# Kernel tuning notes

Measured on AMD Instinct MI355X. Metric: run time of the kernel, lower is better.

## Reference

```python
import jax, jax.numpy as jnp
import numpy as np

Q, C, T = 256, 128, 128
L = Q + C + T            # 512
D = 1024                 # d_model
H = 8                    # heads
DK = D // H              # 128 = self_attn.d_k
F = 3                    # num_latent_relations
R = 50                   # num_relation_kinds = len(relations2id)
FF = 4 * D               # feed-forward hidden
DEFAULT_QQ_ID = 0        # relations2id['q:q-default']
EPS = 1e-5


def setup_inputs():
    key = jax.random.key(0)
    ks = jax.random.split(key, 40)
    s = 0.02
    def nrm(k, shape, scale=s):
        return jax.random.normal(k, shape, jnp.float32) * scale
    inp = {
        'x': jax.random.normal(ks[0], (1, L, D), jnp.float32),
        'qc_relation': jax.random.uniform(ks[1], (Q, C, F), jnp.float32),
        'cq_relation': jax.random.uniform(ks[2], (C, Q, F), jnp.float32),
        'qt_relation': jax.random.uniform(ks[3], (Q, T, F), jnp.float32),
        'tq_relation': jax.random.uniform(ks[4], (T, Q, F), jnp.float32),
        'ct_relation': jax.random.randint(ks[5], (C + T, C + T), 0, R, jnp.int32),
        'predefined_relation': jax.random.randint(ks[6], (L, L), 0, R, jnp.int32),
        'mask': jnp.ones((1, L, L), jnp.int32),
        # relation embedding tables
        'rel_k_emb': nrm(ks[7], (R, DK)), 'rel_v_emb': nrm(ks[8], (R, DK)),
        'lqc_k': nrm(ks[9], (F, DK)), 'lqc_v': nrm(ks[10], (F, DK)),
        'lcq_k': nrm(ks[11], (F, DK)), 'lcq_v': nrm(ks[12], (F, DK)),
        'lqt_k': nrm(ks[13], (F, DK)), 'lqt_v': nrm(ks[14], (F, DK)),
        'ltq_k': nrm(ks[15], (F, DK)), 'ltq_v': nrm(ks[16], (F, DK)),
        # attention projections (torch Linear: y = x @ W.T + b)
        'Wq': nrm(ks[17], (D, D)), 'bq': jnp.zeros((D,), jnp.float32),
        'Wk': nrm(ks[18], (D, D)), 'bk': jnp.zeros((D,), jnp.float32),
        'Wv': nrm(ks[19], (D, D)), 'bv': jnp.zeros((D,), jnp.float32),
        'Wo': nrm(ks[20], (D, D)), 'bo': jnp.zeros((D,), jnp.float32),
        # layer norms
        'ln1_g': jnp.ones((D,), jnp.float32), 'ln1_b': jnp.zeros((D,), jnp.float32),
        'ln2_g': jnp.ones((D,), jnp.float32), 'ln2_b': jnp.zeros((D,), jnp.float32),
        # FFN
        'W1': nrm(ks[21], (FF, D)), 'b1': jnp.zeros((FF,), jnp.float32),
        'W2': nrm(ks[22], (D, FF)), 'b2': jnp.zeros((D,), jnp.float32),
    }
    return inp


def layer_norm(x, g, b):
    m = jnp.mean(x, -1, keepdims=True)
    v = jnp.mean((x - m) ** 2, -1, keepdims=True)
    return (x - m) * jax.lax.rsqrt(v + EPS) * g + b


def build_latent_relation(ct, qc, cq, qt, tq, emb, lqc, lcq, lqt, ltq):
    # qq block: every entry is the default-qq embedding row
    qq = jnp.broadcast_to(emb[DEFAULT_QQ_ID], (Q, Q, DK))
    qc_e = jnp.einsum('qcf,fd->qcd', qc, lqc)
    cq_e = jnp.einsum('cqf,fd->cqd', cq, lcq)
    qt_e = jnp.einsum('qtf,fd->qtd', qt, lqt)
    tq_e = jnp.einsum('tqf,fd->tqd', tq, ltq)
    ct_e = emb[ct]                                      # [(c+t),(c+t),DK]
    top = jnp.concatenate([qq, qc_e, qt_e], axis=1)      # [Q, L, DK]
    bot = jnp.concatenate([jnp.concatenate([cq_e, tq_e], 0), ct_e], axis=1)  # [C+T, L, DK]
    return jnp.concatenate([top, bot], axis=0)           # [L, L, DK]


def relation_attention(x, rel_k, rel_v, mask, Wq, bq, Wk, bk, Wv, bv, Wo, bo):
    B = x.shape[0]
    def proj(W, b):
        return (x @ W.T + b).reshape(B, L, H, DK).transpose(0, 2, 1, 3)  # [B,H,L,DK]
    q, k, v = proj(Wq, bq), proj(Wk, bk), proj(Wv, bv)
    scores = (jnp.einsum('bhid,bhjd->bhij', q, k)
              + jnp.einsum('bhid,ijd->bhij', q, rel_k)) / jnp.sqrt(jnp.float32(DK))
    scores = jnp.where(mask[:, None] == 0, jnp.float32(-1e9), scores)
    p = jax.nn.softmax(scores, axis=-1)
    o = (jnp.einsum('bhij,bhjd->bhid', p, v)
         + jnp.einsum('bhij,ijd->bhid', p, rel_v))
    o = o.transpose(0, 2, 1, 3).reshape(B, L, D)
    return o @ Wo.T + bo


def reference(x, qc_relation, cq_relation, qt_relation, tq_relation,
              ct_relation, predefined_relation, mask,
              rel_k_emb, rel_v_emb, lqc_k, lqc_v, lcq_k, lcq_v,
              lqt_k, lqt_v, ltq_k, ltq_v,
              Wq, bq, Wk, bk, Wv, bv, Wo, bo,
              ln1_g, ln1_b, ln2_g, ln2_b, W1, b1, W2, b2):
    # latent relation build + combine with predefined lookup
    rel_k = (rel_k_emb[predefined_relation]
             + build_latent_relation(ct_relation, qc_relation, cq_relation,
                                     qt_relation, tq_relation,
                                     rel_k_emb, lqc_k, lcq_k, lqt_k, ltq_k))
    rel_v = (rel_v_emb[predefined_relation]
             + build_latent_relation(ct_relation, qc_relation, cq_relation,
                                     qt_relation, tq_relation,
                                     rel_v_emb, lqc_v, lcq_v, lqt_v, ltq_v))
    # sublayer 0: pre-norm relation-biased self attention (dropout=0)
    h = x + relation_attention(layer_norm(x, ln1_g, ln1_b), rel_k, rel_v, mask,
                               Wq, bq, Wk, bk, Wv, bv, Wo, bo)
    # sublayer 1: pre-norm FFN
    y = layer_norm(h, ln2_g, ln2_b)
    ffn = jax.nn.relu(y @ W1.T + b1) @ W2.T + b2
    return h + ffn
```

## Files before the change

### kernel.cpp

```cpp
#include <hip/hip_runtime.h>
#include <hip/hip_bf16.h>

#define LL 512
#define DD 1024
#define HH 8
#define DKK 128
#define QQ 256
#define CCC 128
#define TTT 128
#define RR 50
#define FFF 4096

typedef __attribute__((ext_vector_type(8))) short short8;
typedef __attribute__((ext_vector_type(4))) float float4v;

__device__ __forceinline__ unsigned short f2bu(float f) {
  __hip_bfloat16 h = __float2bfloat16(f);
  unsigned short u; __builtin_memcpy(&u, &h, 2); return u;
}
__device__ __forceinline__ float b2f(unsigned short u) {
  unsigned int v = ((unsigned int)u) << 16;
  float f; __builtin_memcpy(&f, &v, 4); return f;
}
__device__ __forceinline__ int4 cvt8(float4 x, float4 y) {
  int4 o;
  o.x = (int)f2bu(x.x) | ((int)f2bu(x.y) << 16);
  o.y = (int)f2bu(x.z) | ((int)f2bu(x.w) << 16);
  o.z = (int)f2bu(y.x) | ((int)f2bu(y.y) << 16);
  o.w = (int)f2bu(y.z) | ((int)f2bu(y.w) << 16);
  return o;
}

__device__ __forceinline__ void lds_barrier() {
  __builtin_amdgcn_sched_barrier(0);
  __builtin_amdgcn_s_waitcnt(0xC07F);
  __builtin_amdgcn_s_barrier();
  __builtin_amdgcn_sched_barrier(0);
}

#define LOADSET(A0,A1,B0,B1,F0,F1,F2,F3,itv) { int k0v = (itv) << 6;          \
  A0 = *(const int4*)(Az + (size_t)(bm + r)*lda + k0v + gc*8);                \
  A1 = *(const int4*)(Az + (size_t)(bm + 32 + r)*lda + k0v + gc*8);           \
  if constexpr (!CONVB) {                                                     \
    B0 = *(const int4*)(Bz16 + (size_t)(bnb + r)*ldb + k0v + gc*8);           \
    if constexpr (NB > 1)                                                     \
      B1 = *(const int4*)(Bz16 + (size_t)(bnb + 32 + r)*ldb + k0v + gc*8);    \
  } else {                                                                    \
    F0 = *(const float4*)(Bz32 + (size_t)(bnb + r)*ldb + k0v + gc*8);         \
    F1 = *(const float4*)(Bz32 + (size_t)(bnb + r)*ldb + k0v + gc*8 + 4);     \
    if constexpr (NB > 1) {                                                   \
      F2 = *(const float4*)(Bz32 + (size_t)(bnb + 32 + r)*ldb + k0v + gc*8);  \
      F3 = *(const float4*)(Bz32 + (size_t)(bnb + 32 + r)*ldb + k0v + gc*8 + 4); } } }

#define STORESET2(basep,A0,A1,B0,B1,F0,F1,F2,F3) {                            \
  char* bse = (basep);                                                        \
  *(int4*)(bse + r*128 + sl*16) = A0;                                         \
  *(int4*)(bse + (32 + r)*128 + sl*16) = A1;                                  \
  if constexpr (!CONVB) {                                                     \
    *(int4*)(bse + ABYTES + r*128 + sl*16) = B0;                              \
    if constexpr (NB > 1)                                                     \
      *(int4*)(bse + ABYTES + (32 + r)*128 + sl*16) = B1;                     \
  } else {                                                                    \
    *(int4*)(bse + ABYTES + r*128 + sl*16) = cvt8(F0, F1);                    \
    if constexpr (NB > 1)                                                     \
      *(int4*)(bse + ABYTES + (32 + r)*128 + sl*16) = cvt8(F2, F3); } }

__global__ __launch_bounds__(256) void ln_bf16_kernel(const float* __restrict__ x,
    const float* __restrict__ g, const float* __restrict__ b,
    unsigned short* __restrict__ y)
{
  int row = blockIdx.x, t = threadIdx.x;
  const float4 xv = ((const float4*)(x + row*DD))[t];
  float s  = xv.x+xv.y+xv.z+xv.w;
  float ss = xv.x*xv.x+xv.y*xv.y+xv.z*xv.z+xv.w*xv.w;
  __shared__ float rs[256], rss[256];
  rs[t]=s; rss[t]=ss; __syncthreads();
  for (int st=128; st>0; st>>=1){ if (t<st){ rs[t]+=rs[t+st]; rss[t]+=rss[t+st]; } __syncthreads(); }
  float mean = rs[0] * (1.0f/DD);
  float var  = rss[0]*(1.0f/DD) - mean*mean;
  float inv  = rsqrtf(var + 1e-5f);
  float4 gv = ((const float4*)g)[t], bv = ((const float4*)b)[t];
  ushort4 ov;
  ov.x = f2bu((xv.x-mean)*inv*gv.x + bv.x);
  ov.y = f2bu((xv.y-mean)*inv*gv.y + bv.y);
  ov.z = f2bu((xv.z-mean)*inv*gv.z + bv.z);
  ov.w = f2bu((xv.w-mean)*inv*gv.w + bv.w);
  ((ushort4*)(y + row*DD))[t] = ov;
}

__global__ __launch_bounds__(256) void ln_bf16_addb_kernel(float* __restrict__ x,
    const float* __restrict__ g, const float* __restrict__ b,
    const float* __restrict__ b2, unsigned short* __restrict__ y)
{
  int row = blockIdx.x, t = threadIdx.x;
  const float4 xv = ((const float4*)(x + row*DD))[t];
  float s  = xv.x+xv.y+xv.z+xv.w;
  float ss = xv.x*xv.x+xv.y*xv.y+xv.z*xv.z+xv.w*xv.w;
  __shared__ float rs[256], rss[256];
  rs[t]=s; rss[t]=ss; __syncthreads();
  for (int st=128; st>0; st>>=1){ if (t<st){ rs[t]+=rs[t+st]; rss[t]+=rss[t+st]; } __syncthreads(); }
  float mean = rs[0] * (1.0f/DD);
  float var  = rss[0]*(1.0f/DD) - mean*mean;
  float inv  = rsqrtf(var + 1e-5f);
  float4 gv = ((const float4*)g)[t], bv = ((const float4*)b)[t];
  ushort4 ov;
  ov.x = f2bu((xv.x-mean)*inv*gv.x + bv.x);
  ov.y = f2bu((xv.y-mean)*inv*gv.y + bv.y);
  ov.z = f2bu((xv.z-mean)*inv*gv.z + bv.z);
  ov.w = f2bu((xv.w-mean)*inv*gv.w + bv.w);
  ((ushort4*)(y + row*DD))[t] = ov;
  float4 b2v = ((const float4*)b2)[t];
  float4 nx; nx.x = xv.x+b2v.x; nx.y = xv.y+b2v.y; nx.z = xv.z+b2v.z; nx.w = xv.w+b2v.w;
  ((float4*)(x + row*DD))[t] = nx;
}

template<int BN, int CONVB, int ZK, int OUT_BF16, int RELU, int HAS_SRC, int HAS_BIAS>
__global__ __launch_bounds__(256) void gemm_pl(
    const unsigned short* __restrict__ A, int lda, size_t sAz,
    const void* __restrict__ Bv, int ldb, size_t sBz,
    const float* __restrict__ bias,
    const float* __restrict__ src, int ldsrc, size_t sSz,
    void* __restrict__ Cv, int ldc, size_t sCz,
    int K)
{
  constexpr int BM = 64;
  constexpr int WM = 32, WN = BN/2, FM = 2, FN = WN/16;
  constexpr int NB = BN/32;
  constexpr int ABYTES = BM*128, TILE = ABYTES + BN*128;
  __shared__ char lds[2*TILE];
  int t = threadIdx.x, w = t >> 6, l = t & 63;
  size_t z = blockIdx.z;
  const unsigned short* Az = A + z*sAz;
  const unsigned short* Bz16 = (const unsigned short*)Bv + (CONVB ? 0 : z*sBz);
  const float*          Bz32 = (const float*)Bv + (CONVB ? z*sBz : 0);
  int bm = blockIdx.y*BM, bn = blockIdx.x*BN;
  int bnb = bn;
  int wm = (w>>1)*WM, wn = (w&1)*WN;

  float4v acc[FM][FN];
  #pragma unroll
  for (int m=0;m<FM;++m)
    #pragma unroll
    for (int n=0;n<FN;++n) acc[m][n] = (float4v){0.f,0.f,0.f,0.f};

  int r = t >> 3, sl = t & 7;
  int gc = sl ^ (r & 7);
  int quad = l >> 4, lrow = l & 15;
  const int nit = K >> 6;

  int4 pa0, pa1, pb0, pb1;  float4 pf0, pf1, pf2, pf3;
  int4 qa0, qa1, qb0, qb1;  float4 qf0, qf1, qf2, qf3;

  auto compute = [&](const char* base) {
    const char* ab = base;
    const char* bb = base + ABYTES;
    #pragma unroll
    for (int step=0; step<2; ++step) {
      int c = step*4 + quad;
      short8 af[FM], bf[FN];
      #pragma unroll
      for (int m=0;m<FM;++m) {
        int Rw = wm + m*16 + lrow;
        af[m] = *(const short8*)(ab + Rw*128 + ((c ^ (Rw & 7))*16));
      }
      #pragma unroll
      for (int n=0;n<FN;++n) {
        int Rw = wn + n*16 + lrow;
        bf[n] = *(const short8*)(bb + Rw*128 + ((c ^ (Rw & 7))*16));
      }
      #pragma unroll
      for (int m=0;m<FM;++m)
        #pragma unroll
        for (int n=0;n<FN;++n)
          acc[m][n] = __builtin_amdgcn_mfma_f32_16x16x32_bf16(af[m], bf[n], acc[m][n], 0, 0, 0);
    }
  };

  LOADSET(pa0,pa1,pb0,pb1,pf0,pf1,pf2,pf3, 0);
  LOADSET(qa0,qa1,qb0,qb1,qf0,qf1,qf2,qf3, 1);
  for (int it = 0; it < nit; it += 2) {
    STORESET2(lds, pa0,pa1,pb0,pb1,pf0,pf1,pf2,pf3);
    if (it + 2 < nit) LOADSET(pa0,pa1,pb0,pb1,pf0,pf1,pf2,pf3, it+2);
    lds_barrier();
    compute(lds);
    STORESET2(lds + TILE, qa0,qa1,qb0,qb1,qf0,qf1,qf2,qf3);
    if (it + 3 < nit) LOADSET(qa0,qa1,qb0,qb1,qf0,qf1,qf2,qf3, it+3);
    lds_barrier();
    compute(lds + TILE);
  }

  #pragma unroll
  for (int m=0;m<FM;++m)
    #pragma unroll
    for (int n=0;n<FN;++n)
      #pragma unroll
      for (int rg=0;rg<4;++rg) {
        int row = bm + wm + m*16 + quad*4 + rg;
        int col = bn + wn + n*16 + lrow;
        float vv = acc[m][n][rg];
        if (ZK) {
          atomicAdd(&((float*)Cv)[(size_t)row*ldc + col], vv);
        } else {
          if (HAS_BIAS) vv += bias[col];
          if (HAS_SRC)  vv += src[z*sSz + (size_t)row*ldsrc + col];
          if (RELU) vv = fmaxf(vv, 0.f);
          if (OUT_BF16) ((unsigned short*)Cv)[z*sCz + (size_t)row*ldc + col] = f2bu(vv);
          else          ((float*)Cv)[z*sCz + (size_t)row*ldc + col] = vv;
        }
      }
}

__global__ __launch_bounds__(256) void gemm_qkv_pl(
    const unsigned short* __restrict__ A,
    const float* __restrict__ Wq, const float* __restrict__ Wk,
    const float* __restrict__ Wv,
    const float* __restrict__ bq, const float* __restrict__ bk,
    const float* __restrict__ bv,
    unsigned short* __restrict__ Qh, unsigned short* __restrict__ Kh,
    unsigned short* __restrict__ Vt)
{
  constexpr int BN = 64, CONVB = 1;
  constexpr int WM = 32, WN = 32, FM = 2, FN = 2;
  constexpr int NB = 2;
  constexpr int ABYTES = 64*128, TILE = ABYTES + BN*128;
  __shared__ char lds[2*TILE];
  int t = threadIdx.x, w = t >> 6, l = t & 63;
  int bm = blockIdx.y*64, bn = blockIdx.x*BN;
  int wm = (w>>1)*WM, wn = (w&1)*WN;
  const int lda = DD, ldb = DD, nit = DD >> 6;
  const unsigned short* Az = A;
  int part0 = bn >> 10;
  const float* Bz32 = (part0==0 ? Wq : part0==1 ? Wk : Wv) + (size_t)(bn & 1023)*DD;
  const unsigned short* Bz16 = nullptr; (void)Bz16;
  int bnb = 0;

  float4v acc[FM][FN];
  #pragma unroll
  for (int m=0;m<FM;++m)
    #pragma unroll
    for (int n=0;n<FN;++n) acc[m][n] = (float4v){0.f,0.f,0.f,0.f};

  int r = t >> 3, sl = t & 7;
  int gc = sl ^ (r & 7);
  int quad = l >> 4, lrow = l & 15;

  int4 pa0, pa1, pb0, pb1;  float4 pf0, pf1, pf2, pf3;
  int4 qa0, qa1, qb0, qb1;  float4 qf0, qf1, qf2, qf3;

  auto compute = [&](const char* base) {
    const char* ab = base;
    const char* bb = base + ABYTES;
    #pragma unroll
    for (int step=0; step<2; ++step) {
      int c = step*4 + quad;
      short8 af[FM], bf[FN];
      #pragma unroll
      for (int m=0;m<FM;++m) {
        int Rw = wm + m*16 + lrow;
        af[m] = *(const short8*)(ab + Rw*128 + ((c ^ (Rw & 7))*16));
      }
      #pragma unroll
      for (int n=0;n<FN;++n) {
        int Rw = wn + n*16 + lrow;
        bf[n] = *(const short8*)(bb + Rw*128 + ((c ^ (Rw & 7))*16));
      }
      #pragma unroll
      for (int m=0;m<FM;++m)
        #pragma unroll
        for (int n=0;n<FN;++n)
          acc[m][n] = __builtin_amdgcn_mfma_f32_16x16x32_bf16(af[m], bf[n], acc[m][n], 0, 0, 0);
    }
  };

  LOADSET(pa0,pa1,pb0,pb1,pf0,pf1,pf2,pf3, 0);
  LOADSET(qa0,qa1,qb0,qb1,qf0,qf1,qf2,qf3, 1);
  for (int it = 0; it < nit; it += 2) {
    STORESET2(lds, pa0,pa1,pb0,pb1,pf0,pf1,pf2,pf3);
    if (it + 2 < nit) LOADSET(pa0,pa1,pb0,pb1,pf0,pf1,pf2,pf3, it+2);
    lds_barrier();
    compute(lds);
    STORESET2(lds + TILE, qa0,qa1,qb0,qb1,qf0,qf1,qf2,qf3);
    if (it + 3 < nit) LOADSET(qa0,qa1,qb0,qb1,qf0,qf1,qf2,qf3, it+3);
    lds_barrier();
    compute(lds + TILE);
  }

  #pragma unroll
  for (int m=0;m<FM;++m)
    #pragma unroll
    for (int n=0;n<FN;++n)
      #pragma unroll
      for (int rg=0;rg<4;++rg) {
        int row = bm + wm + m*16 + quad*4 + rg;
        int col = bn + wn + n*16 + lrow;
        int part = col >> 10, hh = (col >> 7) & 7, d = col & 127;
        const float* bp = (part==0) ? bq : (part==1) ? bk : bv;
        float vv = acc[m][n][rg] + bp[col & 1023];
        unsigned short o = f2bu(vv);
        if (part == 0)      Qh[((size_t)hh*LL + row)*DKK + d] = o;
        else if (part == 1) Kh[((size_t)hh*LL + row)*DKK + d] = o;
        else                Vt[((size_t)hh*DKK + d)*LL + row] = o;
      }
}

__global__ __launch_bounds__(64) void qtab_kernel(const unsigned short* __restrict__ Qh,
    const float* __restrict__ embk,
    const float* __restrict__ lqc, const float* __restrict__ lqt,
    const float* __restrict__ lcq, const float* __restrict__ ltq,
    float* __restrict__ qe, float* __restrict__ ql)
{
  int i = blockIdx.x, h = blockIdx.y, t = threadIdx.x;
  __shared__ float qrow[128];
  const unsigned short* qp = Qh + ((size_t)h*LL + i)*DKK;
  qrow[t] = b2f(qp[t]); qrow[t+64] = b2f(qp[t+64]);
  __syncthreads();
  if (t < RR) {
    float s = 0.f;
    #pragma unroll 8
    for (int d=0; d<128; ++d) s += qrow[d]*embk[t*128+d];
    qe[(i*HH+h)*RR + t] = s;
  } else if (t < RR + 12) {
    int u = t - RR;
    int tb = u/3, f = u - tb*3;
    const float* tab = (tb==0) ? lqc : (tb==1) ? lqt : (tb==2) ? lcq : ltq;
    const float* tr = tab + f*128;
    float s = 0.f;
    #pragma unroll 8
    for (int d=0; d<128; ++d) s += qrow[d]*tr[d];
    ql[((tb*LL + i)*HH + h)*3 + f] = s;
  }
}

__global__ __launch_bounds__(512) void softmax_pw_kernel(
    float* __restrict__ S,
    const float* __restrict__ qe, const float* __restrict__ ql,
    const float* __restrict__ qcr, const float* __restrict__ cqr,
    const float* __restrict__ qtr, const float* __restrict__ tqr,
    const int* __restrict__ ct,   const int* __restrict__ pred,
    const int* __restrict__ mask,
    const float* __restrict__ embv,
    const float* __restrict__ lqc_v, const float* __restrict__ lcq_v,
    const float* __restrict__ lqt_v, const float* __restrict__ ltq_v,
    float* __restrict__ o2)
{
  int i = blockIdx.x, h = blockIdx.y, j = threadIdx.x;
  int w = j >> 6;
  __shared__ float qerow[52];
  __shared__ float pws[52];
  __shared__ float pf1s[3], pf2s[3];
  __shared__ float redw[8], redw2[8];
  if (j < RR) qerow[j] = qe[(i*HH+h)*RR + j];
  if (j >= 64 && j < 64+52) pws[j-64] = 0.f;
  if (j >= 192 && j < 195) pf1s[j-192] = 0.f;
  if (j >= 256 && j < 259) pf2s[j-256] = 0.f;

  float lq1[3] = {0,0,0}, lq2[3] = {0,0,0};
  if (i < QQ) {
    #pragma unroll
    for (int f=0; f<3; ++f) {
      lq1[f] = ql[((0*LL + i)*HH + h)*3 + f];
      lq2[f] = ql[((1*LL + i)*HH + h)*3 + f];
    }
  } else if (i < QQ+CCC) {
    #pragma unroll
    for (int f=0; f<3; ++f) lq1[f] = ql[((2*LL + i)*HH + h)*3 + f];
  } else {
    #pragma unroll
    for (int f=0; f<3; ++f) lq1[f] = ql[((3*LL + i)*HH + h)*3 + f];
  }

  float c0=0.f, c1=0.f, c2=0.f; int route; int scat2 = 0;
  if (i < QQ) {
    if (j < QQ) { route = 0; scat2 = 0; }
    else if (j < QQ+CCC) { const float* rr = qcr + (i*CCC + (j-QQ))*3;
      c0=rr[0]; c1=rr[1]; c2=rr[2]; route = 1; }
    else { const float* rr = qtr + (i*TTT + (j-QQ-CCC))*3;
      c0=rr[0]; c1=rr[1]; c2=rr[2]; route = 2; }
  } else {
    if (j < QQ) { const float* rr = (i < QQ+CCC) ? cqr + ((i-QQ)*QQ + j)*3
                                                 : tqr + ((i-QQ-CCC)*QQ + j)*3;
      c0=rr[0]; c1=rr[1]; c2=rr[2]; route = 1; }
    else { route = 0; scat2 = ct[(i-QQ)*(CCC+TTT) + (j-QQ)]; }
  }
  int predv = pred[i*LL + j];
  float s = S[((size_t)h*LL + i)*LL + j];
  __syncthreads();

  s += qerow[predv];
  if (route == 0)      s += qerow[scat2];
  else if (route == 1) s += c0*lq1[0] + c1*lq1[1] + c2*lq1[2];
  else                 s += c0*lq2[0] + c1*lq2[1] + c2*lq2[2];
  s *= 0.08838834764831845f;
  if (mask[i*LL + j] == 0) s = -1e9f;

  float m = s;
  #pragma unroll
  for (int off=32; off>=1; off>>=1) m = fmaxf(m, __shfl_xor(m, off));
  if ((j & 63) == 0) redw[w] = m;
  __syncthreads();
  float mx = redw[0];
  #pragma unroll
  for (int k=1; k<8; ++k) mx = fmaxf(mx, redw[k]);

  float e = __expf(s - mx);
  float sm = e;
  #pragma unroll
  for (int off=32; off>=1; off>>=1) sm += __shfl_xor(sm, off);
  if ((j & 63) == 0) redw2[w] = sm;
  __syncthreads();
  float tot = 0.f;
  #pragma unroll
  for (int k=0; k<8; ++k) tot += redw2[k];
  float p = e * (1.0f/tot);

  ((unsigned short*)S)[((size_t)h*LL + i)*1024 + j] = f2bu(p);

  atomicAdd(&pws[predv], p);
  if (route == 0) atomicAdd(&pws[scat2], p);
  float f10=0.f,f11=0.f,f12=0.f,f20=0.f,f21=0.f,f22=0.f;
  if (route == 1) { f10=p*c0; f11=p*c1; f12=p*c2; }
  else if (route == 2) { f20=p*c0; f21=p*c1; f22=p*c2; }
  #pragma unroll
  for (int off=32; off>=1; off>>=1) {
    f10 += __shfl_xor(f10, off); f11 += __shfl_xor(f11, off); f12 += __shfl_xor(f12, off);
    f20 += __shfl_xor(f20, off); f21 += __shfl_xor(f21, off); f22 += __shfl_xor(f22, off);
  }
  if ((j & 63) == 0) {
    atomicAdd(&pf1s[0], f10); atomicAdd(&pf1s[1], f11); atomicAdd(&pf1s[2], f12);
    atomicAdd(&pf2s[0], f20); atomicAdd(&pf2s[1], f21); atomicAdd(&pf2s[2], f22);
  }
  __syncthreads();

  if (j < 128) {
    const float* tab1; const float* tab2 = nullptr;
    if (i < QQ)          { tab1 = lqc_v; tab2 = lqt_v; }
    else if (i < QQ+CCC) { tab1 = lcq_v; }
    else                 { tab1 = ltq_v; }
    int d = j;
    float acc = 0.f;
    #pragma unroll 5
    for (int r = 0; r < RR; ++r) acc += pws[r]*embv[r*128 + d];
    acc += pf1s[0]*tab1[d] + pf1s[1]*tab1[128+d] + pf1s[2]*tab1[256+d];
    if (tab2) acc += pf2s[0]*tab2[d] + pf2s[1]*tab2[128+d] + pf2s[2]*tab2[256+d];
    o2[((size_t)h*LL + i)*DKK + d] = acc;
  }
}

extern "C" void kernel_launch(void* const* d_in, const int* in_sizes, int n_in,
                              void* d_out, int out_size, void* d_ws, size_t ws_size,
                              hipStream_t stream)
{
  const float* x    = (const float*)d_in[0];
  const float* qcr  = (const float*)d_in[1];
  const float* cqr  = (const float*)d_in[2];
  const float* qtr  = (const float*)d_in[3];
  const float* tqr  = (const float*)d_in[4];
  const int*   ct   = (const int*)d_in[5];
  const int*   pred = (const int*)d_in[6];
  const int*   mask = (const int*)d_in[7];
  const float* embk = (const float*)d_in[8];
  const float* embv = (const float*)d_in[9];
  const float* lqc_k = (const float*)d_in[10];
  const float* lqc_v = (const float*)d_in[11];
  const float* lcq_k = (const float*)d_in[12];
  const float* lcq_v = (const float*)d_in[13];
  const float* lqt_k = (const float*)d_in[14];
  const float* lqt_v = (const float*)d_in[15];
  const float* ltq_k = (const float*)d_in[16];
  const float* ltq_v = (const float*)d_in[17];
  const float* Wq = (const float*)d_in[18]; const float* bq = (const float*)d_in[19];
  const float* Wk = (const float*)d_in[20]; const float* bk = (const float*)d_in[21];
  const float* Wv = (const float*)d_in[22]; const float* bv = (const float*)d_in[23];
  const float* Wo = (const float*)d_in[24]; const float* bo = (const float*)d_in[25];
  const float* ln1_g = (const float*)d_in[26]; const float* ln1_b = (const float*)d_in[27];
  const float* ln2_g = (const float*)d_in[28]; const float* ln2_b = (const float*)d_in[29];
  const float* W1 = (const float*)d_in[30]; const float* b1 = (const float*)d_in[31];
  const float* W2 = (const float*)d_in[32]; const float* b2 = (const float*)d_in[33];
  float* out = (float*)d_out;

  float* wsf = (float*)d_ws;
  float* S    = wsf;
  float* o2   = S + (size_t)HH*LL*LL;
  float* qe   = o2 + (size_t)HH*LL*DKK;
  float* ql   = qe + LL*HH*RR;
  unsigned short* ub = (unsigned short*)(ql + 4*LL*HH*3);
  unsigned short* ybuf_b = ub;
  unsigned short* obuf_b = ybuf_b + LL*DD;
  unsigned short* Qh     = obuf_b + LL*DD;
  unsigned short* Kh     = Qh + LL*DD;
  unsigned short* Vt     = Kh + LL*DD;
  unsigned short* PS     = (unsigned short*)S;
  unsigned short* hidden = (unsigned short*)S;

  ln_bf16_kernel<<<LL, 256, 0, stream>>>(x, ln1_g, ln1_b, ybuf_b);
  gemm_qkv_pl<<<dim3(48, 8), 256, 0, stream>>>(ybuf_b, Wq, Wk, Wv, bq, bk, bv,
                                               Qh, Kh, Vt);
  qtab_kernel<<<dim3(LL, HH), 64, 0, stream>>>(Qh, embk, lqc_k, lqt_k, lcq_k, ltq_k, qe, ql);
  gemm_pl<64,0,0,0,0,0,0><<<dim3(8, 8, 8), 256, 0, stream>>>(
      Qh, DKK, (size_t)LL*DKK, Kh, DKK, (size_t)LL*DKK,
      nullptr, nullptr, 0, 0, S, LL, (size_t)LL*LL, DKK);
  softmax_pw_kernel<<<dim3(LL, HH), 512, 0, stream>>>(
      S, qe, ql, qcr, cqr, qtr, tqr, ct, pred, mask,
      embv, lqc_v, lcq_v, lqt_v, ltq_v, o2);
  gemm_pl<32,0,0,1,0,1,0><<<dim3(4, 8, 8), 256, 0, stream>>>(
      PS, 1024, (size_t)LL*1024, Vt, LL, (size_t)DKK*LL,
      nullptr, o2, DKK, (size_t)LL*DKK, obuf_b, DD, (size_t)DKK, LL);
  gemm_pl<32,1,0,0,0,1,1><<<dim3(32, 8, 1), 256, 0, stream>>>(
      obuf_b, DD, 0, Wo, DD, 0, bo, x, DD, 0, out, DD, 0, DD);
  ln_bf16_addb_kernel<<<LL, 256, 0, stream>>>(out, ln2_g, ln2_b, b2, ybuf_b);
  gemm_pl<64,1,0,1,1,0,1><<<dim3(64, 8, 1), 256, 0, stream>>>(
      ybuf_b, DD, 0, W1, DD, 0, b1, nullptr, 0, 0, hidden, FFF, 0, DD);
  gemm_pl<64,1,1,0,0,0,0><<<dim3(16, 8, 4), 256, 0, stream>>>(
      hidden, FFF, (size_t)1024, W2, FFF, (size_t)1024,
      nullptr, nullptr, 0, 0, out, DD, 0, 1024);
}
```

Before: 276.7 us.

## Fold relation-key tables into QK GEMM, batch heads in softmax, deepen prefetch

Appends the relation key embedding and latent tables as 64 extra rows of each head's K buffer, so the QK^T GEMM also produces the q·emb scores. This removes the separate qtab kernel and its qe/ql buffers. The softmax kernel now handles all 8 heads per row in one block, which amortises the pred/mask/relation loads across heads. Most GEMMs also get a 4-deep register prefetch pipeline, at the cost of more registers and a changed workspace layout (padded S/PS strides).

```diff
diff --git a/kernel.cpp b/kernel.cpp
--- a/kernel.cpp
+++ b/kernel.cpp
@@ -10,6 +10,9 @@
 #define TTT 128
 #define RR 50
 #define FFF 4096
+#define KLD 576
+#define SLD 576
+#define PLD 1152
 
 typedef __attribute__((ext_vector_type(8))) short short8;
 typedef __attribute__((ext_vector_type(4))) float float4v;
@@ -64,6 +67,25 @@
     *(int4*)(bse + ABYTES + r*128 + sl*16) = cvt8(F0, F1);                    \
     if constexpr (NB > 1)                                                     \
       *(int4*)(bse + ABYTES + (32 + r)*128 + sl*16) = cvt8(F2, F3); } }
+
+__global__ __launch_bounds__(256) void kprep_kernel(
+    const float* __restrict__ embk,
+    const float* __restrict__ lqc, const float* __restrict__ lqt,
+    const float* __restrict__ lcq, const float* __restrict__ ltq,
+    unsigned short* __restrict__ Kh)
+{
+  int g = blockIdx.x*256 + threadIdx.x;
+  if (g >= 8*64*128) return;
+  int d = g & 127, rr = (g >> 7) & 63, h = g >> 13;
+  float v = 0.f;
+  if (rr < 50) v = embk[rr*128 + d];
+  else if (rr < 62) {
+    int u = rr - 50; int tb = u/3, f = u - tb*3;
+    const float* tab = (tb==0) ? lqc : (tb==1) ? lqt : (tb==2) ? lcq : ltq;
+    v = tab[f*128 + d];
+  }
+  Kh[((size_t)h*KLD + 512 + rr)*DKK + d] = f2bu(v);
+}
 
 __global__ __launch_bounds__(256) void ln_bf16_kernel(const float* __restrict__ x,
     const float* __restrict__ g, const float* __restrict__ b,
@@ -114,7 +136,7 @@
   ((float4*)(x + row*DD))[t] = nx;
 }
 
-template<int BN, int CONVB, int ZK, int OUT_BF16, int RELU, int HAS_SRC, int HAS_BIAS>
+template<int BN, int DEPTH, int CONVB, int ZK, int OUT_BF16, int RELU, int HAS_SRC, int HAS_BIAS>
 __global__ __launch_bounds__(256) void gemm_pl(
     const unsigned short* __restrict__ A, int lda, size_t sAz,
     const void* __restrict__ Bv, int ldb, size_t sBz,
@@ -148,8 +170,10 @@
   int quad = l >> 4, lrow = l & 15;
   const int nit = K >> 6;
 
-  int4 pa0, pa1, pb0, pb1;  float4 pf0, pf1, pf2, pf3;
-  int4 qa0, qa1, qb0, qb1;  float4 qf0, qf1, qf2, qf3;
+  int4 Aa0, Aa1, Ab0, Ab1;  float4 Af0, Af1, Af2, Af3;
+  int4 Ba0, Ba1, Bb0, Bb1;  float4 Bf0, Bf1, Bf2, Bf3;
+  int4 Ca0, Ca1, Cb0, Cb1;  float4 Cf0, Cf1, Cf2, Cf3;
+  int4 Da0, Da1, Db0, Db1;  float4 Df0, Df1, Df2, Df3;
 
   auto compute = [&](const char* base) {
     const char* ab = base;
@@ -176,17 +200,42 @@
     }
   };
 
-  LOADSET(pa0,pa1,pb0,pb1,pf0,pf1,pf2,pf3, 0);
-  LOADSET(qa0,qa1,qb0,qb1,qf0,qf1,qf2,qf3, 1);
-  for (int it = 0; it < nit; it += 2) {
-    STORESET2(lds, pa0,pa1,pb0,pb1,pf0,pf1,pf2,pf3);
-    if (it + 2 < nit) LOADSET(pa0,pa1,pb0,pb1,pf0,pf1,pf2,pf3, it+2);
-    lds_barrier();
-    compute(lds);
-    STORESET2(lds + TILE, qa0,qa1,qb0,qb1,qf0,qf1,qf2,qf3);
-    if (it + 3 < nit) LOADSET(qa0,qa1,qb0,qb1,qf0,qf1,qf2,qf3, it+3);
-    lds_barrier();
-    compute(lds + TILE);
+  if constexpr (DEPTH == 2) {
+    LOADSET(Aa0,Aa1,Ab0,Ab1,Af0,Af1,Af2,Af3, 0);
+    LOADSET(Ba0,Ba1,Bb0,Bb1,Bf0,Bf1,Bf2,Bf3, 1);
+    for (int it = 0; it < nit; it += 2) {
+      STORESET2(lds, Aa0,Aa1,Ab0,Ab1,Af0,Af1,Af2,Af3);
+      if (it + 2 < nit) LOADSET(Aa0,Aa1,Ab0,Ab1,Af0,Af1,Af2,Af3, it+2);
+      lds_barrier();
+      compute(lds);
+      STORESET2(lds + TILE, Ba0,Ba1,Bb0,Bb1,Bf0,Bf1,Bf2,Bf3);
+      if (it + 3 < nit) LOADSET(Ba0,Ba1,Bb0,Bb1,Bf0,Bf1,Bf2,Bf3, it+3);
+      lds_barrier();
+      compute(lds + TILE);
+    }
+  } else {
+    LOADSET(Aa0,Aa1,Ab0,Ab1,Af0,Af1,Af2,Af3, 0);
+    LOADSET(Ba0,Ba1,Bb0,Bb1,Bf0,Bf1,Bf2,Bf3, 1);
+    LOADSET(Ca0,Ca1,Cb0,Cb1,Cf0,Cf1,Cf2,Cf3, 2);
+    LOADSET(Da0,Da1,Db0,Db1,Df0,Df1,Df2,Df3, 3);
+    for (int it = 0; it < nit; it += 4) {
+      STORESET2(lds, Aa0,Aa1,Ab0,Ab1,Af0,Af1,Af2,Af3);
+      if (it + 4 < nit) LOADSET(Aa0,Aa1,Ab0,Ab1,Af0,Af1,Af2,Af3, it+4);
+      lds_barrier();
+      compute(lds);
+      STORESET2(lds + TILE, Ba0,Ba1,Bb0,Bb1,Bf0,Bf1,Bf2,Bf3);
+      if (it + 5 < nit) LOADSET(Ba0,Ba1,Bb0,Bb1,Bf0,Bf1,Bf2,Bf3, it+5);
+      lds_barrier();
+      compute(lds + TILE);
+      STORESET2(lds, Ca0,Ca1,Cb0,Cb1,Cf0,Cf1,Cf2,Cf3);
+      if (it + 6 < nit) LOADSET(Ca0,Ca1,Cb0,Cb1,Cf0,Cf1,Cf2,Cf3, it+6);
+      lds_barrier();
+      compute(lds);
+      STORESET2(lds + TILE, Da0,Da1,Db0,Db1,Df0,Df1,Df2,Df3);
+      if (it + 7 < nit) LOADSET(Da0,Da1,Db0,Db1,Df0,Df1,Df2,Df3, it+7);
+      lds_barrier();
+      compute(lds + TILE);
+    }
   }
 
   #pragma unroll
@@ -244,8 +293,10 @@
   int gc = sl ^ (r & 7);
   int quad = l >> 4, lrow = l & 15;
 
-  int4 pa0, pa1, pb0, pb1;  float4 pf0, pf1, pf2, pf3;
-  int4 qa0, qa1, qb0, qb1;  float4 qf0, qf1, qf2, qf3;
+  int4 Aa0, Aa1, Ab0, Ab1;  float4 Af0, Af1, Af2, Af3;
+  int4 Ba0, Ba1, Bb0, Bb1;  float4 Bf0, Bf1, Bf2, Bf3;
+  int4 Ca0, Ca1, Cb0, Cb1;  float4 Cf0, Cf1, Cf2, Cf3;
+  int4 Da0, Da1, Db0, Db1;  float4 Df0, Df1, Df2, Df3;
 
   auto compute = [&](const char* base) {
     const char* ab = base;
@@ -272,15 +323,25 @@
     }
   };
 
-  LOADSET(pa0,pa1,pb0,pb1,pf0,pf1,pf2,pf3, 0);
-  LOADSET(qa0,qa1,qb0,qb1,qf0,qf1,qf2,qf3, 1);
-  for (int it = 0; it < nit; it += 2) {
-    STORESET2(lds, pa0,pa1,pb0,pb1,pf0,pf1,pf2,pf3);
-    if (it + 2 < nit) LOADSET(pa0,pa1,pb0,pb1,pf0,pf1,pf2,pf3, it+2);
+  LOADSET(Aa0,Aa1,Ab0,Ab1,Af0,Af1,Af2,Af3, 0);
+  LOADSET(Ba0,Ba1,Bb0,Bb1,Bf0,Bf1,Bf2,Bf3, 1);
+  LOADSET(Ca0,Ca1,Cb0,Cb1,Cf0,Cf1,Cf2,Cf3, 2);
+  LOADSET(Da0,Da1,Db0,Db1,Df0,Df1,Df2,Df3, 3);
+  for (int it = 0; it < nit; it += 4) {
+    STORESET2(lds, Aa0,Aa1,Ab0,Ab1,Af0,Af1,Af2,Af3);
+    if (it + 4 < nit) LOADSET(Aa0,Aa1,Ab0,Ab1,Af0,Af1,Af2,Af3, it+4);
     lds_barrier();
     compute(lds);
-    STORESET2(lds + TILE, qa0,qa1,qb0,qb1,qf0,qf1,qf2,qf3);
-    if (it + 3 < nit) LOADSET(qa0,qa1,qb0,qb1,qf0,qf1,qf2,qf3, it+3);
+    STORESET2(lds + TILE, Ba0,Ba1,Bb0,Bb1,Bf0,Bf1,Bf2,Bf3);
+    if (it + 5 < nit) LOADSET(Ba0,Ba1,Bb0,Bb1,Bf0,Bf1,Bf2,Bf3, it+5);
+    lds_barrier();
+    compute(lds + TILE);
+    STORESET2(lds, Ca0,Ca1,Cb0,Cb1,Cf0,Cf1,Cf2,Cf3);
+    if (it + 6 < nit) LOADSET(Ca0,Ca1,Cb0,Cb1,Cf0,Cf1,Cf2,Cf3, it+6);
+    lds_barrier();
+    compute(lds);
+    STORESET2(lds + TILE, Da0,Da1,Db0,Db1,Df0,Df1,Df2,Df3);
+    if (it + 7 < nit) LOADSET(Da0,Da1,Db0,Db1,Df0,Df1,Df2,Df3, it+7);
     lds_barrier();
     compute(lds + TILE);
   }
@@ -298,42 +359,13 @@
         float vv = acc[m][n][rg] + bp[col & 1023];
         unsigned short o = f2bu(vv);
         if (part == 0)      Qh[((size_t)hh*LL + row)*DKK + d] = o;
-        else if (part == 1) Kh[((size_t)hh*LL + row)*DKK + d] = o;
+        else if (part == 1) Kh[((size_t)hh*KLD + row)*DKK + d] = o;
         else                Vt[((size_t)hh*DKK + d)*LL + row] = o;
       }
-}
-
-__global__ __launch_bounds__(64) void qtab_kernel(const unsigned short* __restrict__ Qh,
-    const float* __restrict__ embk,
-    const float* __restrict__ lqc, const float* __restrict__ lqt,
-    const float* __restrict__ lcq, const float* __restrict__ ltq,
-    float* __restrict__ qe, float* __restrict__ ql)
-{
-  int i = blockIdx.x, h = blockIdx.y, t = threadIdx.x;
-  __shared__ float qrow[128];
-  const unsigned short* qp = Qh + ((size_t)h*LL + i)*DKK;
-  qrow[t] = b2f(qp[t]); qrow[t+64] = b2f(qp[t+64]);
-  __syncthreads();
-  if (t < RR) {
-    float s = 0.f;
-    #pragma unroll 8
-    for (int d=0; d<128; ++d) s += qrow[d]*embk[t*128+d];
-    qe[(i*HH+h)*RR + t] = s;
-  } else if (t < RR + 12) {
-    int u = t - RR;
-    int tb = u/3, f = u - tb*3;
-    const float* tab = (tb==0) ? lqc : (tb==1) ? lqt : (tb==2) ? lcq : ltq;
-    const float* tr = tab + f*128;
-    float s = 0.f;
-    #pragma unroll 8
-    for (int d=0; d<128; ++d) s += qrow[d]*tr[d];
-    ql[((tb*LL + i)*HH + h)*3 + f] = s;
-  }
 }
 
 __global__ __launch_bounds__(512) void softmax_pw_kernel(
     float* __restrict__ S,
-    const float* __restrict__ qe, const float* __restrict__ ql,
     const float* __restrict__ qcr, const float* __restrict__ cqr,
     const float* __restrict__ qtr, const float* __restrict__ tqr,
     const int* __restrict__ ct,   const int* __restrict__ pred,
@@ -343,32 +375,27 @@
     const float* __restrict__ lqt_v, const float* __restrict__ ltq_v,
     float* __restrict__ o2)
 {
-  int i = blockIdx.x, h = blockIdx.y, j = threadIdx.x;
-  int w = j >> 6;
-  __shared__ float qerow[52];
-  __shared__ float pws[52];
-  __shared__ float pf1s[3], pf2s[3];
-  __shared__ float redw[8], redw2[8];
-  if (j < RR) qerow[j] = qe[(i*HH+h)*RR + j];
-  if (j >= 64 && j < 64+52) pws[j-64] = 0.f;
-  if (j >= 192 && j < 195) pf1s[j-192] = 0.f;
-  if (j >= 256 && j < 259) pf2s[j-256] = 0.f;
-
-  float lq1[3] = {0,0,0}, lq2[3] = {0,0,0};
-  if (i < QQ) {
-    #pragma unroll
-    for (int f=0; f<3; ++f) {
-      lq1[f] = ql[((0*LL + i)*HH + h)*3 + f];
-      lq2[f] = ql[((1*LL + i)*HH + h)*3 + f];
-    }
-  } else if (i < QQ+CCC) {
-    #pragma unroll
-    for (int f=0; f<3; ++f) lq1[f] = ql[((2*LL + i)*HH + h)*3 + f];
-  } else {
-    #pragma unroll
-    for (int f=0; f<3; ++f) lq1[f] = ql[((3*LL + i)*HH + h)*3 + f];
-  }
-
+  int i = blockIdx.x, j = threadIdx.x, w = j >> 6;
+  __shared__ float qerow8[8][52];
+  __shared__ float lq1s[8][3], lq2s[8][3];
+  __shared__ float pws[8][52];
+  __shared__ float pf1s[8][3], pf2s[8][3];
+  __shared__ float redm[8][8], reds[8][8];
+
+  for (int k = j; k < 8*52; k += 512) ((float*)pws)[k] = 0.f;
+  if (j < 24) { ((float*)pf1s)[j] = 0.f; ((float*)pf2s)[j] = 0.f; }
+  if (j < 400) {
+    int h = j / 50, rr = j - h*50;
+    qerow8[h][rr] = S[((size_t)(h*LL + i))*SLD + 512 + rr];
+  } else if (j >= 448 && j < 472) {
+    int u = j - 448; int h = u / 3, f = u - h*3;
+    int base = (i < QQ) ? 562 : (i < QQ+CCC) ? 568 : 571;
+    lq1s[h][f] = S[((size_t)(h*LL + i))*SLD + base + f];
+    lq2s[h][f] = (i < QQ) ? S[((size_t)(h*LL + i))*SLD + 565 + f] : 0.f;
+  }
+
+  int predv = pred[i*LL + j];
+  int maskv = mask[i*LL + j];
   float c0=0.f, c1=0.f, c2=0.f; int route; int scat2 = 0;
   if (i < QQ) {
     if (j < QQ) { route = 0; scat2 = 0; }
@@ -382,67 +409,118 @@
       c0=rr[0]; c1=rr[1]; c2=rr[2]; route = 1; }
     else { route = 0; scat2 = ct[(i-QQ)*(CCC+TTT) + (j-QQ)]; }
   }
-  int predv = pred[i*LL + j];
-  float s = S[((size_t)h*LL + i)*LL + j];
+
+  float sv[8];
+  #pragma unroll
+  for (int h=0; h<8; ++h) sv[h] = S[((size_t)(h*LL + i))*SLD + j];
   __syncthreads();
 
-  s += qerow[predv];
-  if (route == 0)      s += qerow[scat2];
-  else if (route == 1) s += c0*lq1[0] + c1*lq1[1] + c2*lq1[2];
-  else                 s += c0*lq2[0] + c1*lq2[1] + c2*lq2[2];
-  s *= 0.08838834764831845f;
-  if (mask[i*LL + j] == 0) s = -1e9f;
-
-  float m = s;
-  #pragma unroll
-  for (int off=32; off>=1; off>>=1) m = fmaxf(m, __shfl_xor(m, off));
-  if ((j & 63) == 0) redw[w] = m;
+  #pragma unroll
+  for (int h=0; h<8; ++h) {
+    float s = sv[h] + qerow8[h][predv];
+    if (route == 0)      s += qerow8[h][scat2];
+    else if (route == 1) s += c0*lq1s[h][0] + c1*lq1s[h][1] + c2*lq1s[h][2];
+    else                 s += c0*lq2s[h][0] + c1*lq2s[h][1] + c2*lq2s[h][2];
+    s *= 0.08838834764831845f;
+    if (maskv == 0) s = -1e9f;
+    sv[h] = s;
+  }
+
+  float mv[8];
+  #pragma unroll
+  for (int h=0; h<8; ++h) mv[h] = sv[h];
+  #pragma unroll
+  for (int off=32; off>=1; off>>=1) {
+    #pragma unroll
+    for (int h=0; h<8; ++h) mv[h] = fmaxf(mv[h], __shfl_xor(mv[h], off));
+  }
+  if ((j & 63) == 0) {
+    #pragma unroll
+    for (int h=0; h<8; ++h) redm[h][w] = mv[h];
+  }
   __syncthreads();
-  float mx = redw[0];
-  #pragma unroll
-  for (int k=1; k<8; ++k) mx = fmaxf(mx, redw[k]);
-
-  float e = __expf(s - mx);
-  float sm = e;
-  #pragma unroll
-  for (int off=32; off>=1; off>>=1) sm += __shfl_xor(sm, off);
-  if ((j & 63) == 0) redw2[w] = sm;
+  float ev[8];
+  #pragma unroll
+  for (int h=0; h<8; ++h) {
+    float mx = redm[h][0];
+    #pragma unroll
+    for (int k=1; k<8; ++k) mx = fmaxf(mx, redm[h][k]);
+    ev[h] = __expf(sv[h] - mx);
+  }
+  float sm[8];
+  #pragma unroll
+  for (int h=0; h<8; ++h) sm[h] = ev[h];
+  #pragma unroll
+  for (int off=32; off>=1; off>>=1) {
+    #pragma unroll
+    for (int h=0; h<8; ++h) sm[h] += __shfl_xor(sm[h], off);
+  }
+  if ((j & 63) == 0) {
+    #pragma unroll
+    for (int h=0; h<8; ++h) reds[h][w] = sm[h];
+  }
   __syncthreads();
-  float tot = 0.f;
-  #pragma unroll
-  for (int k=0; k<8; ++k) tot += redw2[k];
-  float p = e * (1.0f/tot);
-
-  ((unsigned short*)S)[((size_t)h*LL + i)*1024 + j] = f2bu(p);
-
-  atomicAdd(&pws[predv], p);
-  if (route == 0) atomicAdd(&pws[scat2], p);
-  float f10=0.f,f11=0.f,f12=0.f,f20=0.f,f21=0.f,f22=0.f;
-  if (route == 1) { f10=p*c0; f11=p*c1; f12=p*c2; }
-  else if (route == 2) { f20=p*c0; f21=p*c1; f22=p*c2; }
-  #pragma unroll
-  for (int off=32; off>=1; off>>=1) {
-    f10 += __shfl_xor(f10, off); f11 += __shfl_xor(f11, off); f12 += __shfl_xor(f12, off);
-    f20 += __shfl_xor(f20, off); f21 += __shfl_xor(f21, off); f22 += __shfl_xor(f22, off);
-  }
-  if ((j & 63) == 0) {
-    atomicAdd(&pf1s[0], f10); atomicAdd(&pf1s[1], f11); atomicAdd(&pf1s[2], f12);
-    atomicAdd(&pf2s[0], f20); atomicAdd(&pf2s[1], f21); atomicAdd(&pf2s[2], f22);
+  float pv[8];
+  #pragma unroll
+  for (int h=0; h<8; ++h) {
+    float tot = 0.f;
+    #pragma unroll
+    for (int k=0; k<8; ++k) tot += reds[h][k];
+    pv[h] = ev[h] * (1.0f/tot);
+    ((unsigned short*)S)[((size_t)(h*LL + i))*PLD + j] = f2bu(pv[h]);
+    atomicAdd(&pws[h][predv], pv[h]);
+    if (route == 0) atomicAdd(&pws[h][scat2], pv[h]);
+  }
+  if (route == 1) {
+    #pragma unroll
+    for (int h=0; h<8; ++h) {
+      float f0 = pv[h]*c0, f1 = pv[h]*c1, f2 = pv[h]*c2;
+      #pragma unroll
+      for (int off=32; off>=1; off>>=1) {
+        f0 += __shfl_xor(f0, off); f1 += __shfl_xor(f1, off); f2 += __shfl_xor(f2, off);
+      }
+      if ((j & 63) == 0) {
+        atomicAdd(&pf1s[h][0], f0); atomicAdd(&pf1s[h][1], f1); atomicAdd(&pf1s[h][2], f2);
+      }
+    }
+  } else if (route == 2) {
+    #pragma unroll
+    for (int h=0; h<8; ++h) {
+      float f0 = pv[h]*c0, f1 = pv[h]*c1, f2 = pv[h]*c2;
+      #pragma unroll
+      for (int off=32; off>=1; off>>=1) {
+        f0 += __shfl_xor(f0, off); f1 += __shfl_xor(f1, off); f2 += __shfl_xor(f2, off);
+      }
+      if ((j & 63) == 0) {
+        atomicAdd(&pf2s[h][0], f0); atomicAdd(&pf2s[h][1], f1); atomicAdd(&pf2s[h][2], f2);
+      }
+    }
   }
   __syncthreads();
 
-  if (j < 128) {
+  {
+    int h0 = j >> 7;
+    int d  = j & 127;
     const float* tab1; const float* tab2 = nullptr;
     if (i < QQ)          { tab1 = lqc_v; tab2 = lqt_v; }
     else if (i < QQ+CCC) { tab1 = lcq_v; }
     else                 { tab1 = ltq_v; }
-    int d = j;
-    float acc = 0.f;
+    float accA = 0.f, accB = 0.f;
     #pragma unroll 5
-    for (int r = 0; r < RR; ++r) acc += pws[r]*embv[r*128 + d];
-    acc += pf1s[0]*tab1[d] + pf1s[1]*tab1[128+d] + pf1s[2]*tab1[256+d];
-    if (tab2) acc += pf2s[0]*tab2[d] + pf2s[1]*tab2[128+d] + pf2s[2]*tab2[256+d];
-    o2[((size_t)h*LL + i)*DKK + d] = acc;
+    for (int rr = 0; rr < RR; ++rr) {
+      float evv = embv[rr*128 + d];
+      accA += pws[h0][rr]*evv; accB += pws[h0+4][rr]*evv;
+    }
+    float t0 = tab1[d], t1 = tab1[128+d], t2 = tab1[256+d];
+    accA += pf1s[h0][0]*t0 + pf1s[h0][1]*t1 + pf1s[h0][2]*t2;
+    accB += pf1s[h0+4][0]*t0 + pf1s[h0+4][1]*t1 + pf1s[h0+4][2]*t2;
+    if (tab2) {
+      float u0 = tab2[d], u1 = tab2[128+d], u2 = tab2[256+d];
+      accA += pf2s[h0][0]*u0 + pf2s[h0][1]*u1 + pf2s[h0][2]*u2;
+      accB += pf2s[h0+4][0]*u0 + pf2s[h0+4][1]*u1 + pf2s[h0+4][2]*u2;
+    }
+    o2[((size_t)(h0*LL) + i)*DKK + d] = accA;
+    o2[((size_t)((h0+4)*LL) + i)*DKK + d] = accB;
   }
 }
 
@@ -480,37 +558,36 @@
 
   float* wsf = (float*)d_ws;
   float* S    = wsf;
-  float* o2   = S + (size_t)HH*LL*LL;
-  float* qe   = o2 + (size_t)HH*LL*DKK;
-  float* ql   = qe + LL*HH*RR;
-  unsigned short* ub = (unsigned short*)(ql + 4*LL*HH*3);
+  float* o2   = S + (size_t)HH*LL*SLD;
+  unsigned short* ub = (unsigned short*)(o2 + (size_t)HH*LL*DKK);
   unsigned short* ybuf_b = ub;
   unsigned short* obuf_b = ybuf_b + LL*DD;
   unsigned short* Qh     = obuf_b + LL*DD;
-  unsigned short* Kh     = Qh + LL*DD;
-  unsigned short* Vt     = Kh + LL*DD;
+  unsigned short* Kh     = Qh + (size_t)HH*LL*DKK;
+  unsigned short* Vt     = Kh + (size_t)HH*KLD*DKK;
   unsigned short* PS     = (unsigned short*)S;
   unsigned short* hidden = (unsigned short*)S;
 
+  kprep_kernel<<<(8*64*128 + 255)/256, 256, 0, stream>>>(
+      embk, lqc_k, lqt_k, lcq_k, ltq_k, Kh);
   ln_bf16_kernel<<<LL, 256, 0, stream>>>(x, ln1_g, ln1_b, ybuf_b);
   gemm_qkv_pl<<<dim3(48, 8), 256, 0, stream>>>(ybuf_b, Wq, Wk, Wv, bq, bk, bv,
                                                Qh, Kh, Vt);
-  qtab_kernel<<<dim3(LL, HH), 64, 0, stream>>>(Qh, embk, lqc_k, lqt_k, lcq_k, ltq_k, qe, ql);
-  gemm_pl<64,0,0,0,0,0,0><<<dim3(8, 8, 8), 256, 0, stream>>>(
-      Qh, DKK, (size_t)LL*DKK, Kh, DKK, (size_t)LL*DKK,
-      nullptr, nullptr, 0, 0, S, LL, (size_t)LL*LL, DKK);
-  softmax_pw_kernel<<<dim3(LL, HH), 512, 0, stream>>>(
-      S, qe, ql, qcr, cqr, qtr, tqr, ct, pred, mask,
+  gemm_pl<64,2,0,0,0,0,0,0><<<dim3(9, 8, 8), 256, 0, stream>>>(
+      Qh, DKK, (size_t)LL*DKK, Kh, DKK, (size_t)KLD*DKK,
+      nullptr, nullptr, 0, 0, S, SLD, (size_t)LL*SLD, DKK);
+  softmax_pw_kernel<<<LL, 512, 0, stream>>>(
+      S, qcr, cqr, qtr, tqr, ct, pred, mask,
       embv, lqc_v, lcq_v, lqt_v, ltq_v, o2);
-  gemm_pl<32,0,0,1,0,1,0><<<dim3(4, 8, 8), 256, 0, stream>>>(
-      PS, 1024, (size_t)LL*1024, Vt, LL, (size_t)DKK*LL,
+  gemm_pl<32,4,0,0,1,0,1,0><<<dim3(4, 8, 8), 256, 0, stream>>>(
+      PS, PLD, (size_t)LL*PLD, Vt, LL, (size_t)DKK*LL,
       nullptr, o2, DKK, (size_t)LL*DKK, obuf_b, DD, (size_t)DKK, LL);
-  gemm_pl<32,1,0,0,0,1,1><<<dim3(32, 8, 1), 256, 0, stream>>>(
+  gemm_pl<32,4,1,0,0,0,1,1><<<dim3(32, 8, 1), 256, 0, stream>>>(
       obuf_b, DD, 0, Wo, DD, 0, bo, x, DD, 0, out, DD, 0, DD);
   ln_bf16_addb_kernel<<<LL, 256, 0, stream>>>(out, ln2_g, ln2_b, b2, ybuf_b);
-  gemm_pl<64,1,0,1,1,0,1><<<dim3(64, 8, 1), 256, 0, stream>>>(
+  gemm_pl<64,4,1,0,1,1,0,1><<<dim3(64, 8, 1), 256, 0, stream>>>(
       ybuf_b, DD, 0, W1, DD, 0, b1, nullptr, 0, 0, hidden, FFF, 0, DD);
-  gemm_pl<64,1,1,0,0,0,0><<<dim3(16, 8, 4), 256, 0, stream>>>(
+  gemm_pl<64,4,1,1,0,0,0,0><<<dim3(16, 8, 4), 256, 0, stream>>>(
       hidden, FFF, (size_t)1024, W2, FFF, (size_t)1024,
       nullptr, nullptr, 0, 0, out, DD, 0, 1024);
 }
```

Result: faster. 244.9 us (-11.5%).
